# Performance work log

Hardware: AMD Instinct MI355X
Metric: run time of the kernel (lower is better)

The kernel has to match this reference:

```python
import jax, jax.numpy as jnp
import numpy as np

L, B, E, H = 512, 4, 512, 8
D = E // H  # head_dim = 64


def setup_inputs() -> dict:
    key = jax.random.key(0)
    ks = jax.random.split(key, 7)
    query = jax.random.normal(ks[0], (L, B, E), dtype=jnp.float32)
    relation_k = jax.random.normal(ks[1], (B, L, L, D), dtype=jnp.float32)
    relation_v = jax.random.normal(ks[2], (B, L, L, D), dtype=jnp.float32)
    # xavier-uniform-ish scale for the fused QKV projection
    lim = float(np.sqrt(6.0 / (3 * E + E)))
    in_proj_weight = jax.random.uniform(ks[3], (3 * E, E), jnp.float32, -lim, lim)
    in_proj_bias = jnp.zeros((3 * E,), jnp.float32)
    lim_o = float(np.sqrt(1.0 / E))
    out_proj_weight = jax.random.uniform(ks[4], (E, E), jnp.float32, -lim_o, lim_o)
    out_proj_bias = jnp.zeros((E,), jnp.float32)
    return {
        "query": query,
        "relation_k": relation_k,
        "relation_v": relation_v,
        "in_proj_weight": in_proj_weight,
        "in_proj_bias": in_proj_bias,
        "out_proj_weight": out_proj_weight,
        "out_proj_bias": out_proj_bias,
    }


def reference(query, relation_k, relation_v, in_proj_weight, in_proj_bias,
              out_proj_weight, out_proj_bias):
    # query == key == value (qkv_same path), shape (L, B, E)
    scaling = float(D) ** -0.5
    qkv = query @ in_proj_weight.T + in_proj_bias          # (L, B, 3E)
    q, k, v = jnp.split(qkv, 3, axis=-1)                   # each (L, B, E)
    q = q * scaling

    def to_bhld(t):  # (L, B, E) -> (B, H, L, D)
        return t.reshape(L, B, H, D).transpose(1, 2, 0, 3)

    q, k, v = to_bhld(q), to_bhld(k), to_bhld(v)

    # content scores
    scores = jnp.einsum('bhid,bhjd->bhij', q, k)           # (B, H, L, L)

    # relation_k term: torch does a flat .view of (B*H, L, L, D) -> (B*H*L, D, L)
    # which is a row-major REINTERPRETATION (not a transpose). Replicate via reshape:
    rk = relation_k.reshape(B, L, D, L)                    # per-(b,i) block (L*D,) -> (D, L)
    scores = scores + jnp.einsum('bhid,bidj->bhij', q, rk)

    w = jax.nn.softmax(scores, axis=-1)
    w = jnp.where(jnp.isnan(w), jnp.zeros_like(w), w)      # NaN guard as in original

    out = jnp.einsum('bhij,bhjd->bhid', w, v)              # (B, H, L, D)
    # relation_v term: (B*H*L, 1, L) @ (B*H*L, L, D) -> per-query weighted relation values
    out = out + jnp.einsum('bhij,bijd->bhid', w, relation_v)

    out = out.transpose(2, 0, 1, 3).reshape(L, B, E)       # (B,H,L,D) -> (L,B,E)
    return out @ out_proj_weight.T + out_proj_bias
```

## Files before the change

kernel.cpp:

```cpp
#include <hip/hip_runtime.h>
#include <hip/hip_fp16.h>
#include <stdint.h>


typedef short short8 __attribute__((ext_vector_type(8)));
typedef float f32x4 __attribute__((ext_vector_type(4)));
typedef unsigned short u16x4 __attribute__((ext_vector_type(4)));

static __device__ __forceinline__ uint16_t f2bf(float f) {
  uint32_t u = __float_as_uint(f);
  uint32_t r = (u + 0x7FFFu + ((u >> 16) & 1u)) >> 16;
  return (uint16_t)r;
}
static __device__ __forceinline__ float bf2f(uint16_t h) {
  return __uint_as_float(((uint32_t)h) << 16);
}
static __device__ __forceinline__ short8 ld8(const uint16_t* p) {
  return *(const short8*)p;
}
#define MFMA(a, b, c) __builtin_amdgcn_mfma_f32_16x16x32_bf16((a), (b), (c), 0, 0, 0)

__global__ __launch_bounds__(256) void k_conv_all(
    const float* __restrict__ in_w, const float* __restrict__ query,
    const float* __restrict__ out_w, uint16_t* __restrict__ w_hi,
    uint16_t* __restrict__ w_lo, uint16_t* __restrict__ a_hi,
    uint16_t* __restrict__ a_lo, uint16_t* __restrict__ wo_bf) {
  int e = (blockIdx.x * 256 + threadIdx.x) * 4;
  if (e < 786432) {
    f32x4 v = *(const f32x4*)(in_w + e);
    u16x4 hi, lo;
#pragma unroll
    for (int k = 0; k < 4; ++k) {
      hi[k] = f2bf(v[k]);
      lo[k] = f2bf(v[k] - bf2f(hi[k]));
    }
    *(u16x4*)(w_hi + e) = hi;
    *(u16x4*)(w_lo + e) = lo;
  } else if (e < 786432 + 1048576) {
    int o = e - 786432;
    f32x4 v = *(const f32x4*)(query + o);
    u16x4 hi, lo;
#pragma unroll
    for (int k = 0; k < 4; ++k) {
      hi[k] = f2bf(v[k]);
      lo[k] = f2bf(v[k] - bf2f(hi[k]));
    }
    *(u16x4*)(a_hi + o) = hi;
    *(u16x4*)(a_lo + o) = lo;
  } else {
    int o = e - 1835008;
    f32x4 v = *(const f32x4*)(out_w + o);
    u16x4 hi;
#pragma unroll
    for (int k = 0; k < 4; ++k) hi[k] = f2bf(v[k]);
    *(u16x4*)(wo_bf + o) = hi;
  }
}

__global__ __launch_bounds__(256) void k_inproj(
    const uint16_t* __restrict__ a_hi, const uint16_t* __restrict__ a_lo,
    const uint16_t* __restrict__ w_hi, const uint16_t* __restrict__ w_lo,
    const float* __restrict__ bias, float* __restrict__ q_s,
    uint16_t* __restrict__ q_bf, uint16_t* __restrict__ k_bf,
    uint16_t* __restrict__ v_bf) {
  const int wave = threadIdx.x >> 6, lane = threadIdx.x & 63;
  const int wr = wave >> 1, wc = wave & 1;
  const int rif = lane & 15, kg = lane >> 4;
  const int rbase = blockIdx.x * 64 + wr * 32;
  const int cbase = blockIdx.y * 64 + wc * 32;
  f32x4 acc[2][2] = {};
  for (int ks = 0; ks < 512; ks += 32) {
    int kofs = ks + kg * 8;
    short8 aH[2], aL[2], bH[2], bL[2];
#pragma unroll
    for (int m = 0; m < 2; ++m) {
      size_t idx = (size_t)(rbase + m * 16 + rif) * 512 + kofs;
      aH[m] = ld8(a_hi + idx);
      aL[m] = ld8(a_lo + idx);
    }
#pragma unroll
    for (int n = 0; n < 2; ++n) {
      size_t idx = (size_t)(cbase + n * 16 + rif) * 512 + kofs;
      bH[n] = ld8(w_hi + idx);
      bL[n] = ld8(w_lo + idx);
    }
#pragma unroll
    for (int m = 0; m < 2; ++m)
#pragma unroll
      for (int n = 0; n < 2; ++n) {
        acc[m][n] = MFMA(aH[m], bH[n], acc[m][n]);
        acc[m][n] = MFMA(aH[m], bL[n], acc[m][n]);
        acc[m][n] = MFMA(aL[m], bH[n], acc[m][n]);
      }
  }
#pragma unroll
  for (int m = 0; m < 2; ++m)
#pragma unroll
    for (int n = 0; n < 2; ++n)
#pragma unroll
      for (int r = 0; r < 4; ++r) {
        int row = rbase + m * 16 + kg * 4 + r;
        int col = cbase + n * 16 + rif;
        float val = acc[m][n][r] + bias[col];
        int l = row >> 2, b = row & 3;
        int sel = col >> 9, h = (col >> 6) & 7, d = col & 63;
        size_t oidx = ((size_t)(b * 8 + h) * 512 + l) * 64 + d;
        if (sel == 0) {
          val *= 0.125f;
          q_s[oidx] = val;
          q_bf[oidx] = f2bf(val);
        } else if (sel == 1) {
          k_bf[oidx] = f2bf(val);
        } else {
          v_bf[oidx] = f2bf(val);
        }
      }
}

__global__ __launch_bounds__(256) void k_scores(const uint16_t* __restrict__ q_bf,
                                                const uint16_t* __restrict__ k_bf,
                                                __half* __restrict__ scores) {
  const int bh = blockIdx.x;
  const uint16_t* qb = q_bf + (size_t)bh * 512 * 64;
  const uint16_t* kb = k_bf + (size_t)bh * 512 * 64;
  const int wave = threadIdx.x >> 6, lane = threadIdx.x & 63;
  const int wr = wave >> 1, wc = wave & 1;
  const int rif = lane & 15, kg = lane >> 4;
  const int ibase = blockIdx.y * 64 + wr * 32;
  const int jbase = blockIdx.z * 64 + wc * 32;
  f32x4 acc[2][2] = {};
#pragma unroll
  for (int ks = 0; ks < 64; ks += 32) {
    int kofs = ks + kg * 8;
    short8 A[2], Bb[2];
#pragma unroll
    for (int m = 0; m < 2; ++m) A[m] = ld8(qb + (size_t)(ibase + m * 16 + rif) * 64 + kofs);
#pragma unroll
    for (int n = 0; n < 2; ++n) Bb[n] = ld8(kb + (size_t)(jbase + n * 16 + rif) * 64 + kofs);
#pragma unroll
    for (int m = 0; m < 2; ++m)
#pragma unroll
      for (int n = 0; n < 2; ++n) acc[m][n] = MFMA(A[m], Bb[n], acc[m][n]);
  }
  __half* sc = scores + (size_t)bh * 512 * 512;
#pragma unroll
  for (int m = 0; m < 2; ++m)
#pragma unroll
    for (int n = 0; n < 2; ++n)
#pragma unroll
      for (int r = 0; r < 4; ++r)
        sc[(size_t)(ibase + m * 16 + kg * 4 + r) * 512 + (jbase + n * 16 + rif)] =
            __float2half(acc[m][n][r]);
}

__global__ __launch_bounds__(256) void k_rksm3(
    const float* __restrict__ relation_k, const float* __restrict__ q_s,
    const __half* __restrict__ scores, uint16_t* __restrict__ wprob) {
  __shared__ float qh[512];
  __shared__ float sx[4096];
  const int b = blockIdx.x >> 9, i = blockIdx.x & 511;
  const int t = threadIdx.x;
  const int wave = t >> 6, lane = t & 63;
  for (int e = t; e < 512; e += 256) {
    int h = e >> 6, d = e & 63;
    qh[d * 8 + h] = q_s[(((size_t)b * 8 + h) * 512 + i) * 64 + d];
  }
  __syncthreads();
  const int jq = lane & 31, dh = lane >> 5;
  const int j0 = wave * 128 + jq * 4;
  f32x4 acc[8];
#pragma unroll
  for (int h = 0; h < 8; ++h) acc[h] = f32x4{0.f, 0.f, 0.f, 0.f};
  {
    const float* rkp =
        relation_k + ((size_t)b * 512 + i) * 32768 + (size_t)dh * 32 * 512 + j0;
    const float* qp = qh + dh * 32 * 8;
    for (int dd0 = 0; dd0 < 32; dd0 += 8) {
      f32x4 kv[8];
#pragma unroll
      for (int u = 0; u < 8; ++u)
        kv[u] = __builtin_nontemporal_load((const f32x4*)(rkp + (size_t)(dd0 + u) * 512));
#pragma unroll
      for (int u = 0; u < 8; ++u) {
        f32x4 qA = *(const f32x4*)(qp + (dd0 + u) * 8);
        f32x4 qB = *(const f32x4*)(qp + (dd0 + u) * 8 + 4);
#pragma unroll
        for (int h = 0; h < 4; ++h) {
          acc[h] += qA[h] * kv[u];
          acc[4 + h] += qB[h] * kv[u];
        }
      }
    }
  }
#pragma unroll
  for (int h = 0; h < 8; ++h)
#pragma unroll
    for (int c = 0; c < 4; ++c) acc[h][c] += __shfl_xor(acc[h][c], 32);
  if (dh == 0) {
#pragma unroll
    for (int h = 0; h < 8; ++h) *(f32x4*)&sx[h * 512 + j0] = acc[h];
  }
  __syncthreads();
#pragma unroll
  for (int hh = 0; hh < 2; ++hh) {
    int h = wave * 2 + hh;
    const __half* srow = scores + (((size_t)b * 8 + h) * 512 + i) * 512;
    float s[8], m = -1e30f;
#pragma unroll
    for (int jj = 0; jj < 8; ++jj) {
      int j = jj * 64 + lane;
      s[jj] = __half2float(srow[j]) + sx[h * 512 + j];
      m = fmaxf(m, s[jj]);
    }
    for (int o = 32; o > 0; o >>= 1) m = fmaxf(m, __shfl_xor(m, o));
    float ex[8], sum = 0.f;
#pragma unroll
    for (int jj = 0; jj < 8; ++jj) {
      ex[jj] = __expf(s[jj] - m);
      sum += ex[jj];
    }
    for (int o = 32; o > 0; o >>= 1) sum += __shfl_xor(sum, o);
    float r = 1.f / sum;
    uint16_t* wrow = wprob + (((size_t)b * 8 + h) * 512 + i) * 512;
#pragma unroll
    for (int jj = 0; jj < 8; ++jj) wrow[jj * 64 + lane] = f2bf(ex[jj] * r);
  }
}

__global__ __launch_bounds__(256) void k_pv(const uint16_t* __restrict__ w_bf,
                                            const uint16_t* __restrict__ v_bf,
                                            uint16_t* __restrict__ pv_bf) {
  const int bh = blockIdx.x;
  const int b = bh >> 3, h = bh & 7;
  const uint16_t* wb = w_bf + (size_t)bh * 512 * 512;
  const uint16_t* vb = v_bf + (size_t)bh * 512 * 64;
  const int wave = threadIdx.x >> 6, lane = threadIdx.x & 63;
  const int wr = wave >> 1, wc = wave & 1;
  const int rif = lane & 15, kg = lane >> 4;
  const int ibase = blockIdx.y * 64 + wr * 32;
  const int dbase = wc * 32;
  f32x4 acc[2][2] = {};
  for (int ks = 0; ks < 512; ks += 32) {
    int kofs = ks + kg * 8;
    short8 A[2], Bb[2];
#pragma unroll
    for (int m = 0; m < 2; ++m) A[m] = ld8(wb + (size_t)(ibase + m * 16 + rif) * 512 + kofs);
#pragma unroll
    for (int n = 0; n < 2; ++n) {
      uint16_t tb[8];
#pragma unroll
      for (int e = 0; e < 8; ++e) tb[e] = vb[(size_t)(kofs + e) * 64 + dbase + n * 16 + rif];
      Bb[n] = *(const short8*)tb;
    }
#pragma unroll
    for (int m = 0; m < 2; ++m)
#pragma unroll
      for (int n = 0; n < 2; ++n) acc[m][n] = MFMA(A[m], Bb[n], acc[m][n]);
  }
#pragma unroll
  for (int m = 0; m < 2; ++m)
#pragma unroll
    for (int n = 0; n < 2; ++n)
#pragma unroll
      for (int r = 0; r < 4; ++r) {
        int i = ibase + m * 16 + kg * 4 + r;
        int d = dbase + n * 16 + rif;
        pv_bf[((size_t)i * 4 + b) * 512 + h * 64 + d] = f2bf(acc[m][n][r]);
      }
}

__global__ __launch_bounds__(256) void k_rv2(const float* __restrict__ relation_v,
                                             const uint16_t* __restrict__ wprob,
                                             uint16_t* __restrict__ rv_bf) {
  __shared__ float wT[4608];
  const int b = blockIdx.x >> 9, i = blockIdx.x & 511;
  const int t = threadIdx.x;
  const int wave = t >> 6, lane = t & 63;
  for (int jj = t; jj < 512; jj += 256) {
    uint16_t tmp[8];
#pragma unroll
    for (int h = 0; h < 8; ++h)
      tmp[h] = wprob[(((size_t)b * 8 + h) * 512 + i) * 512 + jj];
#pragma unroll
    for (int h = 0; h < 8; ++h) wT[jj * 9 + h] = bf2f(tmp[h]);
  }
  __syncthreads();
  f32x4 racc[8];
#pragma unroll
  for (int h = 0; h < 8; ++h) racc[h] = f32x4{0.f, 0.f, 0.f, 0.f};
  {
    const int jsub = lane >> 4, d4 = (lane & 15) * 4;
    const float* rvb = relation_v + ((size_t)b * 512 + i) * 32768;
    for (int s8 = 0; s8 < 32; s8 += 8) {
      f32x4 rvv[8];
      int js[8];
#pragma unroll
      for (int u = 0; u < 8; ++u) {
        js[u] = (s8 + u) * 16 + wave * 4 + jsub;
        rvv[u] = *(const f32x4*)(rvb + (size_t)js[u] * 64 + d4);
      }
#pragma unroll
      for (int u = 0; u < 8; ++u) {
        f32x4 w0 = *(const f32x4*)&wT[js[u] * 9];
        f32x4 w1 = *(const f32x4*)&wT[js[u] * 9 + 4];
#pragma unroll
        for (int h = 0; h < 4; ++h) {
          racc[h] += w0[h] * rvv[u];
          racc[4 + h] += w1[h] * rvv[u];
        }
      }
    }
  }
#pragma unroll
  for (int h = 0; h < 8; ++h)
#pragma unroll
    for (int c = 0; c < 4; ++c) {
      racc[h][c] += __shfl_xor(racc[h][c], 16);
      racc[h][c] += __shfl_xor(racc[h][c], 32);
    }
  __syncthreads();
  if (lane < 16) {
#pragma unroll
    for (int h = 0; h < 8; ++h)
      *(f32x4*)&wT[(wave * 8 + h) * 64 + (lane & 15) * 4] = racc[h];
  }
  __syncthreads();
  for (int e = t; e < 512; e += 256) {
    int h = e >> 6, d = e & 63;
    float s = wT[(0 * 8 + h) * 64 + d] + wT[(1 * 8 + h) * 64 + d] +
              wT[(2 * 8 + h) * 64 + d] + wT[(3 * 8 + h) * 64 + d];
    rv_bf[((size_t)i * 4 + b) * 512 + h * 64 + d] = f2bf(s);
  }
}

__global__ __launch_bounds__(256) void k_outproj(const uint16_t* __restrict__ rv_a,
                                                 const uint16_t* __restrict__ pv_a,
                                                 const uint16_t* __restrict__ wo_bf,
                                                 const float* __restrict__ bias,
                                                 float* __restrict__ out) {
  const int wave = threadIdx.x >> 6, lane = threadIdx.x & 63;
  const int wr = wave >> 1, wc = wave & 1;
  const int rif = lane & 15, kg = lane >> 4;
  const int rbase = blockIdx.x * 64 + wr * 32;
  const int cbase = blockIdx.y * 64 + wc * 32;
  f32x4 acc[2][2] = {};
  for (int ks = 0; ks < 512; ks += 32) {
    int kofs = ks + kg * 8;
    short8 A[2], Bb[2];
#pragma unroll
    for (int m = 0; m < 2; ++m) {
      size_t idx = (size_t)(rbase + m * 16 + rif) * 512 + kofs;
      short8 p = ld8(pv_a + idx);
      short8 rr = ld8(rv_a + idx);
      uint16_t tb[8];
#pragma unroll
      for (int e = 0; e < 8; ++e)
        tb[e] = f2bf(bf2f((uint16_t)p[e]) + bf2f((uint16_t)rr[e]));
      A[m] = *(const short8*)tb;
    }
#pragma unroll
    for (int n = 0; n < 2; ++n) Bb[n] = ld8(wo_bf + (size_t)(cbase + n * 16 + rif) * 512 + kofs);
#pragma unroll
    for (int m = 0; m < 2; ++m)
#pragma unroll
      for (int n = 0; n < 2; ++n) acc[m][n] = MFMA(A[m], Bb[n], acc[m][n]);
  }
#pragma unroll
  for (int m = 0; m < 2; ++m)
#pragma unroll
    for (int n = 0; n < 2; ++n)
#pragma unroll
      for (int r = 0; r < 4; ++r) {
        int row = rbase + m * 16 + kg * 4 + r;
        int col = cbase + n * 16 + rif;
        out[(size_t)row * 512 + col] = acc[m][n][r] + bias[col];
      }
}

extern "C" void kernel_launch(void* const* d_in, const int* in_sizes, int n_in,
                              void* d_out, int out_size, void* d_ws, size_t ws_size,
                              hipStream_t stream) {
  const float* query = (const float*)d_in[0];
  const float* relation_k = (const float*)d_in[1];
  const float* relation_v = (const float*)d_in[2];
  const float* in_w = (const float*)d_in[3];
  const float* in_b = (const float*)d_in[4];
  const float* out_w = (const float*)d_in[5];
  const float* out_b = (const float*)d_in[6];
  float* out = (float*)d_out;
  char* ws = (char*)d_ws;

  uint16_t* a_hi  = (uint16_t*)(ws + 0);
  uint16_t* a_lo  = (uint16_t*)(ws + 2097152);
  uint16_t* w_hi  = (uint16_t*)(ws + 4194304);
  uint16_t* w_lo  = (uint16_t*)(ws + 5767168);
  uint16_t* wo_bf = (uint16_t*)(ws + 7340032);
  float*    q_s   = (float*)   (ws + 7864320);
  uint16_t* q_bf  = (uint16_t*)(ws + 12058624);
  uint16_t* k_bf  = (uint16_t*)(ws + 14155776);
  uint16_t* v_bf  = (uint16_t*)(ws + 16252928);
  uint16_t* rv_bf = (uint16_t*)(ws + 18350080);
  uint16_t* pv_bf = (uint16_t*)(ws + 20447232);
  uint16_t* wprob = (uint16_t*)(ws + 22544384);
  __half*   sc_h  = (__half*)  (ws + 39321600);

  k_conv_all<<<dim3(2048), 256, 0, stream>>>(in_w, query, out_w, w_hi, w_lo, a_hi, a_lo, wo_bf);
  k_inproj<<<dim3(32, 24), 256, 0, stream>>>(a_hi, a_lo, w_hi, w_lo, in_b, q_s, q_bf, k_bf, v_bf);
  k_scores<<<dim3(32, 8, 8), 256, 0, stream>>>(q_bf, k_bf, sc_h);
  k_rksm3<<<dim3(2048), 256, 0, stream>>>(relation_k, q_s, sc_h, wprob);
  k_pv<<<dim3(32, 8), 256, 0, stream>>>(wprob, v_bf, pv_bf);
  k_rv2<<<dim3(2048), 256, 0, stream>>>(relation_v, wprob, rv_bf);
  k_outproj<<<dim3(32, 8), 256, 0, stream>>>(rv_bf, pv_bf, wo_bf, out_b, out);
}
```

Measured before the change: 193.4 us.

## Stream relation_k/relation_v through LDS with double-buffered global_load_lds

The relation_k score kernel and the relation_v accumulation kernel now stage their large streaming reads through LDS using direct global-to-LDS loads, double-buffered with explicit vmcnt waits. Each iteration issues one 16-byte load per lane, replacing batches of eight register loads. The relation_v kernel also keeps the probabilities as bf16 in LDS rather than expanding them to fp32. The aim is to overlap memory fetch with the FMA work and reduce register pressure on these bandwidth-bound kernels. The cost is only one load in flight per wave, which may lower memory-level parallelism compared with the previous eight outstanding loads.

```diff
diff --git a/kernel.cpp b/kernel.cpp
--- a/kernel.cpp
+++ b/kernel.cpp
@@ -6,6 +6,9 @@
 typedef short short8 __attribute__((ext_vector_type(8)));
 typedef float f32x4 __attribute__((ext_vector_type(4)));
 typedef unsigned short u16x4 __attribute__((ext_vector_type(4)));
+
+typedef __attribute__((address_space(3))) uint32_t lds_u32;
+typedef __attribute__((address_space(1))) uint32_t glob_u32;
 
 static __device__ __forceinline__ uint16_t f2bf(float f) {
   uint32_t u = __float_as_uint(f);
@@ -17,6 +20,9 @@
 }
 static __device__ __forceinline__ short8 ld8(const uint16_t* p) {
   return *(const short8*)p;
+}
+static __device__ __forceinline__ void gload_lds16(const float* g, float* l) {
+  __builtin_amdgcn_global_load_lds((const glob_u32*)g, (lds_u32*)l, 16, 0, 0);
 }
 #define MFMA(a, b, c) __builtin_amdgcn_mfma_f32_16x16x32_bf16((a), (b), (c), 0, 0, 0)
 
@@ -153,11 +159,11 @@
             __float2half(acc[m][n][r]);
 }
 
-__global__ __launch_bounds__(256) void k_rksm3(
+__global__ __launch_bounds__(256) void k_rksm5(
     const float* __restrict__ relation_k, const float* __restrict__ q_s,
     const __half* __restrict__ scores, uint16_t* __restrict__ wprob) {
   __shared__ float qh[512];
-  __shared__ float sx[4096];
+  __shared__ float sxs[4096];
   const int b = blockIdx.x >> 9, i = blockIdx.x & 511;
   const int t = threadIdx.x;
   const int wave = t >> 6, lane = t & 63;
@@ -168,37 +174,46 @@
   __syncthreads();
   const int jq = lane & 31, dh = lane >> 5;
   const int j0 = wave * 128 + jq * 4;
+  const float* rkb = relation_k + ((size_t)b * 512 + i) * 32768;
   f32x4 acc[8];
 #pragma unroll
   for (int h = 0; h < 8; ++h) acc[h] = f32x4{0.f, 0.f, 0.f, 0.f};
   {
-    const float* rkp =
-        relation_k + ((size_t)b * 512 + i) * 32768 + (size_t)dh * 32 * 512 + j0;
-    const float* qp = qh + dh * 32 * 8;
-    for (int dd0 = 0; dd0 < 32; dd0 += 8) {
-      f32x4 kv[8];
-#pragma unroll
-      for (int u = 0; u < 8; ++u)
-        kv[u] = __builtin_nontemporal_load((const f32x4*)(rkp + (size_t)(dd0 + u) * 512));
-#pragma unroll
-      for (int u = 0; u < 8; ++u) {
-        f32x4 qA = *(const f32x4*)(qp + (dd0 + u) * 8);
-        f32x4 qB = *(const f32x4*)(qp + (dd0 + u) * 8 + 4);
-#pragma unroll
-        for (int h = 0; h < 4; ++h) {
-          acc[h] += qA[h] * kv[u];
-          acc[4 + h] += qB[h] * kv[u];
-        }
-      }
+    auto STAGE = [&](int c, int buf) {
+      const float* g = rkb + (size_t)(2 * c + dh) * 512 + wave * 128 + jq * 4;
+      gload_lds16(g, &sxs[buf * 1024 + wave * 256]);
+    };
+    STAGE(0, 0);
+    int buf = 0;
+#pragma unroll 4
+    for (int c = 0; c < 32; ++c) {
+      if (c < 31) {
+        STAGE(c + 1, buf ^ 1);
+        asm volatile("s_waitcnt vmcnt(1)" ::: "memory");
+      } else {
+        asm volatile("s_waitcnt vmcnt(0)" ::: "memory");
+      }
+      __builtin_amdgcn_sched_barrier(0);
+      int d = 2 * c + dh;
+      f32x4 kv = *(const f32x4*)&sxs[buf * 1024 + wave * 256 + dh * 128 + jq * 4];
+      f32x4 qA = *(const f32x4*)&qh[d * 8];
+      f32x4 qB = *(const f32x4*)&qh[d * 8 + 4];
+#pragma unroll
+      for (int h = 0; h < 4; ++h) {
+        acc[h] += qA[h] * kv;
+        acc[4 + h] += qB[h] * kv;
+      }
+      buf ^= 1;
     }
   }
 #pragma unroll
   for (int h = 0; h < 8; ++h)
 #pragma unroll
     for (int c = 0; c < 4; ++c) acc[h][c] += __shfl_xor(acc[h][c], 32);
+  __syncthreads();
   if (dh == 0) {
 #pragma unroll
-    for (int h = 0; h < 8; ++h) *(f32x4*)&sx[h * 512 + j0] = acc[h];
+    for (int h = 0; h < 8; ++h) *(f32x4*)&sxs[h * 512 + j0] = acc[h];
   }
   __syncthreads();
 #pragma unroll
@@ -209,7 +224,7 @@
 #pragma unroll
     for (int jj = 0; jj < 8; ++jj) {
       int j = jj * 64 + lane;
-      s[jj] = __half2float(srow[j]) + sx[h * 512 + j];
+      s[jj] = __half2float(srow[j]) + sxs[h * 512 + j];
       m = fmaxf(m, s[jj]);
     }
     for (int o = 32; o > 0; o >>= 1) m = fmaxf(m, __shfl_xor(m, o));
@@ -269,46 +284,54 @@
       }
 }
 
-__global__ __launch_bounds__(256) void k_rv2(const float* __restrict__ relation_v,
+__global__ __launch_bounds__(256) void k_rv4(const float* __restrict__ relation_v,
                                              const uint16_t* __restrict__ wprob,
                                              uint16_t* __restrict__ rv_bf) {
-  __shared__ float wT[4608];
+  __shared__ uint16_t wTb[6144];
+  __shared__ float vstage[2048];
   const int b = blockIdx.x >> 9, i = blockIdx.x & 511;
   const int t = threadIdx.x;
   const int wave = t >> 6, lane = t & 63;
   for (int jj = t; jj < 512; jj += 256) {
-    uint16_t tmp[8];
 #pragma unroll
     for (int h = 0; h < 8; ++h)
-      tmp[h] = wprob[(((size_t)b * 8 + h) * 512 + i) * 512 + jj];
-#pragma unroll
-    for (int h = 0; h < 8; ++h) wT[jj * 9 + h] = bf2f(tmp[h]);
-  }
-  __syncthreads();
+      wTb[jj * 12 + h] = wprob[(((size_t)b * 8 + h) * 512 + i) * 512 + jj];
+  }
+  __syncthreads();
+  const int jsub = lane >> 4, d4 = (lane & 15) * 4;
+  const float* rvb = relation_v + ((size_t)b * 512 + i) * 32768;
   f32x4 racc[8];
 #pragma unroll
   for (int h = 0; h < 8; ++h) racc[h] = f32x4{0.f, 0.f, 0.f, 0.f};
   {
-    const int jsub = lane >> 4, d4 = (lane & 15) * 4;
-    const float* rvb = relation_v + ((size_t)b * 512 + i) * 32768;
-    for (int s8 = 0; s8 < 32; s8 += 8) {
-      f32x4 rvv[8];
-      int js[8];
-#pragma unroll
-      for (int u = 0; u < 8; ++u) {
-        js[u] = (s8 + u) * 16 + wave * 4 + jsub;
-        rvv[u] = *(const f32x4*)(rvb + (size_t)js[u] * 64 + d4);
-      }
-#pragma unroll
-      for (int u = 0; u < 8; ++u) {
-        f32x4 w0 = *(const f32x4*)&wT[js[u] * 9];
-        f32x4 w1 = *(const f32x4*)&wT[js[u] * 9 + 4];
-#pragma unroll
-        for (int h = 0; h < 4; ++h) {
-          racc[h] += w0[h] * rvv[u];
-          racc[4 + h] += w1[h] * rvv[u];
-        }
-      }
+    auto STAGE = [&](int c, int buf) {
+      const float* g = rvb + (size_t)(c * 16 + wave * 4 + jsub) * 64 + d4;
+      gload_lds16(g, &vstage[buf * 1024 + wave * 256]);
+    };
+    STAGE(0, 0);
+    int buf = 0;
+#pragma unroll 4
+    for (int c = 0; c < 32; ++c) {
+      if (c < 31) {
+        STAGE(c + 1, buf ^ 1);
+        asm volatile("s_waitcnt vmcnt(1)" ::: "memory");
+      } else {
+        asm volatile("s_waitcnt vmcnt(0)" ::: "memory");
+      }
+      __builtin_amdgcn_sched_barrier(0);
+      int j = c * 16 + wave * 4 + jsub;
+      f32x4 rv4 = *(const f32x4*)&vstage[buf * 1024 + wave * 256 + jsub * 64 + d4];
+      uint2 wlo = *(const uint2*)&wTb[j * 12];
+      uint2 whi = *(const uint2*)&wTb[j * 12 + 4];
+      uint16_t tw[8];
+      *(uint2*)tw = wlo;
+      *(uint2*)(tw + 4) = whi;
+#pragma unroll
+      for (int h = 0; h < 4; ++h) {
+        racc[h] += bf2f(tw[h]) * rv4;
+        racc[4 + h] += bf2f(tw[4 + h]) * rv4;
+      }
+      buf ^= 1;
     }
   }
 #pragma unroll
@@ -322,13 +345,13 @@
   if (lane < 16) {
 #pragma unroll
     for (int h = 0; h < 8; ++h)
-      *(f32x4*)&wT[(wave * 8 + h) * 64 + (lane & 15) * 4] = racc[h];
+      *(f32x4*)&vstage[(wave * 8 + h) * 64 + (lane & 15) * 4] = racc[h];
   }
   __syncthreads();
   for (int e = t; e < 512; e += 256) {
     int h = e >> 6, d = e & 63;
-    float s = wT[(0 * 8 + h) * 64 + d] + wT[(1 * 8 + h) * 64 + d] +
-              wT[(2 * 8 + h) * 64 + d] + wT[(3 * 8 + h) * 64 + d];
+    float s = vstage[(0 * 8 + h) * 64 + d] + vstage[(1 * 8 + h) * 64 + d] +
+              vstage[(2 * 8 + h) * 64 + d] + vstage[(3 * 8 + h) * 64 + d];
     rv_bf[((size_t)i * 4 + b) * 512 + h * 64 + d] = f2bf(s);
   }
 }
@@ -407,8 +430,8 @@
   k_conv_all<<<dim3(2048), 256, 0, stream>>>(in_w, query, out_w, w_hi, w_lo, a_hi, a_lo, wo_bf);
   k_inproj<<<dim3(32, 24), 256, 0, stream>>>(a_hi, a_lo, w_hi, w_lo, in_b, q_s, q_bf, k_bf, v_bf);
   k_scores<<<dim3(32, 8, 8), 256, 0, stream>>>(q_bf, k_bf, sc_h);
-  k_rksm3<<<dim3(2048), 256, 0, stream>>>(relation_k, q_s, sc_h, wprob);
+  k_rksm5<<<dim3(2048), 256, 0, stream>>>(relation_k, q_s, sc_h, wprob);
   k_pv<<<dim3(32, 8), 256, 0, stream>>>(wprob, v_bf, pv_bf);
-  k_rv2<<<dim3(2048), 256, 0, stream>>>(relation_v, wprob, rv_bf);
+  k_rv4<<<dim3(2048), 256, 0, stream>>>(relation_v, wprob, rv_bf);
   k_outproj<<<dim3(32, 8), 256, 0, stream>>>(rv_bf, pv_bf, wo_bf, out_b, out);
 }
```

New measurement: 215.0 us. 1.11x slower.
